# Kernel tuning notes

Measured on AMD Instinct MI355X. Metric: run time of the kernel, lower is better.

## Reference

```python
import jax, jax.numpy as jnp
import numpy as np

LN_EPS = 1e-5

def _layernorm(x, g, b):
    mu = jnp.mean(x, axis=-1, keepdims=True)
    var = jnp.var(x, axis=-1, keepdims=True)
    return (x - mu) * jax.lax.rsqrt(var + LN_EPS) * g + b

def setup_inputs() -> dict:
    key = jax.random.key(0)
    B, S, D, H = 2, 2048, 1024, 16
    dh = D // H          # 64
    r = 48               # r_attn = int(0.75*min(D,dh))
    r_out = 768          # int(0.75*D)
    I = 4 * D            # GPT-2 MLP inner dim
    r_mlp = 512          # int(0.5*min(D,I))
    ks = jax.random.split(key, 24)
    sc = lambda *sh: 0.02
    inp = {
        'hidden_states': jax.random.normal(ks[0], (B, S, D), jnp.float32),
        'ln1_g': jnp.ones((D,), jnp.float32), 'ln1_b': jnp.zeros((D,), jnp.float32),
        'ln2_g': jnp.ones((D,), jnp.float32), 'ln2_b': jnp.zeros((D,), jnp.float32),
        'q_U': jax.random.normal(ks[1], (D, H, r), jnp.float32) * 0.02,
        'q_V': jax.random.normal(ks[2], (H, r, dh), jnp.float32) * 0.02,
        'q_b': jax.random.normal(ks[3], (H, dh), jnp.float32) * 0.02,
        'k_U': jax.random.normal(ks[4], (D, H, r), jnp.float32) * 0.02,
        'k_V': jax.random.normal(ks[5], (H, r, dh), jnp.float32) * 0.02,
        'k_b': jax.random.normal(ks[6], (H, dh), jnp.float32) * 0.02,
        'v_U': jax.random.normal(ks[7], (D, H, r), jnp.float32) * 0.02,
        'v_V': jax.random.normal(ks[8], (H, r, dh), jnp.float32) * 0.02,
        'v_b': jax.random.normal(ks[9], (H, dh), jnp.float32) * 0.02,
        'out_U': jax.random.normal(ks[10], (D, r_out), jnp.float32) * 0.02,
        'out_V': jax.random.normal(ks[11], (r_out, D), jnp.float32) * 0.02,
        'out_b': jnp.zeros((D,), jnp.float32),
        'fc1_U': jax.random.normal(ks[12], (D, r_mlp), jnp.float32) * 0.02,
        'fc1_V': jax.random.normal(ks[13], (r_mlp, I), jnp.float32) * 0.02,
        'fc1_b': jnp.zeros((I,), jnp.float32),
        'fc2_U': jax.random.normal(ks[14], (I, r_mlp), jnp.float32) * 0.02,
        'fc2_V': jax.random.normal(ks[15], (r_mlp, D), jnp.float32) * 0.02,
        'fc2_b': jnp.zeros((D,), jnp.float32),
    }
    return inp

def reference(hidden_states, ln1_g, ln1_b, ln2_g, ln2_b,
              q_U, q_V, q_b, k_U, k_V, k_b, v_U, v_V, v_b,
              out_U, out_V, out_b, fc1_U, fc1_V, fc1_b, fc2_U, fc2_V, fc2_b):
    B, S, D = hidden_states.shape
    H, dh = q_V.shape[0], q_V.shape[2]
    x = _layernorm(hidden_states, ln1_g, ln1_b)
    # low-rank per-head projections (latent P then reconstruct)
    Q = jnp.einsum('bsd,dhr,hre->bhse', x, q_U, q_V) + q_b[None, :, None, :]
    Pk = jnp.einsum('bsd,dhr->bhsr', x, k_U)
    Pv = jnp.einsum('bsd,dhr->bhsr', x, v_U)
    K = jnp.einsum('bhsr,hrd->bhsd', Pk, k_V) + k_b[None, :, None, :]
    V = jnp.einsum('bhsr,hrd->bhsd', Pv, v_V) + v_b[None, :, None, :]
    # causal scaled dot-product attention
    scale = 1.0 / jnp.sqrt(jnp.asarray(dh, x.dtype))
    scores = jnp.einsum('bhse,bhte->bhst', Q, K) * scale
    causal = jnp.tril(jnp.ones((S, S), bool))
    scores = jnp.where(causal[None, None], scores, jnp.asarray(-1e9, scores.dtype))
    attn = jax.nn.softmax(scores, axis=-1)
    ctx = jnp.einsum('bhst,bhtd->bhsd', attn, V)          # [B,H,S,dh]
    ctx = ctx.transpose(0, 2, 1, 3).reshape(B, S, D)
    attn_out = (ctx @ out_U) @ out_V + out_b
    h = hidden_states + attn_out
    # low-rank MLP with GPT-2 gelu (tanh approx)
    x2 = _layernorm(h, ln2_g, ln2_b)
    hmid = jax.nn.gelu((x2 @ fc1_U) @ fc1_V + fc1_b, approximate=True)
    mlp_out = (hmid @ fc2_U) @ fc2_V + fc2_b
    return h + mlp_out
```

## Files before the change

kernel.cpp:

```cpp
#include <hip/hip_runtime.h>
#include <hip/hip_bf16.h>

typedef float f32x4 __attribute__((ext_vector_type(4)));
typedef __bf16 bf16x8 __attribute__((ext_vector_type(8)));
typedef __bf16 bf16x4 __attribute__((ext_vector_type(4)));
typedef unsigned short u16x8 __attribute__((ext_vector_type(8)));
typedef unsigned short u16x4 __attribute__((ext_vector_type(4)));

#define QSCALE 0.180336881f

__device__ __forceinline__ unsigned short f2bf(float f) {
  union { float f; unsigned int u; } v; v.f = f;
  return (unsigned short)((v.u + 0x7FFFu + ((v.u >> 16) & 1u)) >> 16);
}

__device__ __forceinline__ f32x4 mfma16(bf16x8 a, bf16x8 b, f32x4 c) {
  return __builtin_amdgcn_mfma_f32_16x16x32_bf16(a, b, c, 0, 0, 0);
}

__device__ __forceinline__ void gload16(const unsigned short* g, unsigned short* l) {
  __builtin_amdgcn_global_load_lds(
      (const __attribute__((address_space(1))) void*)g,
      (__attribute__((address_space(3))) void*)l, 16, 0, 0);
}


__global__ void concat_bias_k(const float* __restrict__ qb, const float* __restrict__ kb,
                              const float* __restrict__ vb, float* __restrict__ out) {
  const int i = blockIdx.x * 256 + threadIdx.x;
  if (i >= 3072) return;
  const float* s = (i < 1024) ? qb : (i < 2048 ? kb : vb);
  out[i] = s[i & 1023] * (i < 1024 ? QSCALE : 1.0f);
}

__global__ void tcvt_k(const float* __restrict__ in, unsigned short* __restrict__ out,
                       int R, int C) {
  __shared__ float tile[32][33];
  const int x = blockIdx.x * 32 + threadIdx.x;
  const int y0 = blockIdx.y * 32;
#pragma unroll
  for (int i = 0; i < 32; i += 8)
    tile[threadIdx.y + i][threadIdx.x] = in[(size_t)(y0 + threadIdx.y + i) * C + x];
  __syncthreads();
  const int ox = y0 + threadIdx.x;
  const int oy0 = blockIdx.x * 32;
#pragma unroll
  for (int i = 0; i < 32; i += 8)
    out[(size_t)(oy0 + threadIdx.y + i) * R + ox] = f2bf(tile[threadIdx.x][threadIdx.y + i]);
}

__global__ void cvt_k(const float* __restrict__ in, unsigned short* __restrict__ out, int n) {
  const int i = (blockIdx.x * 256 + threadIdx.x) * 4;
  if (i >= n) return;
  const f32x4 v = *(const f32x4*)(in + i);
  u16x4 o;
#pragma unroll
  for (int k = 0; k < 4; ++k) o[k] = f2bf(v[k]);
  *(u16x4*)(out + i) = o;
}

__global__ void vtr_k(const unsigned short* __restrict__ QKV, unsigned short* __restrict__ VT) {
  __shared__ unsigned short tile[32][33];
  const int bh = blockIdx.z, b = bh >> 4, h = bh & 15;
  const int s0 = blockIdx.x * 32, d0 = blockIdx.y * 32;
  const unsigned short* src = QKV + (size_t)b * 2048 * 3072 + 2048 + h * 64;
#pragma unroll
  for (int i = 0; i < 32; i += 8)
    tile[threadIdx.y + i][threadIdx.x] = src[(size_t)(s0 + threadIdx.y + i) * 3072 + d0 + threadIdx.x];
  __syncthreads();
  unsigned short* dst = VT + (size_t)bh * 64 * 2048;
#pragma unroll
  for (int i = 0; i < 32; i += 8)
    dst[(size_t)(d0 + threadIdx.y + i) * 2048 + s0 + threadIdx.x] = tile[threadIdx.x][threadIdx.y + i];
}

__global__ __launch_bounds__(256) void wqkv_pre_k(
    const float* __restrict__ qU, const float* __restrict__ qV,
    const float* __restrict__ kU, const float* __restrict__ kV,
    const float* __restrict__ vU, const float* __restrict__ vV,
    unsigned short* __restrict__ WT) {
  __shared__ float Us[64][48];
  __shared__ float Vs[48][64];
  const int m = blockIdx.y >> 4, h = blockIdx.y & 15;
  const int d0 = blockIdx.x * 64;
  const float* U = (m == 0) ? qU : (m == 1 ? kU : vU);
  const float* V = (m == 0) ? qV : (m == 1 ? kV : vV);
  const float qs = (m == 0) ? QSCALE : 1.0f;
  const int t = threadIdx.x;
  for (int idx = t; idx < 64 * 48; idx += 256) {
    const int d = idx / 48, r = idx - d * 48;
    Us[d][r] = U[(size_t)(d0 + d) * 768 + h * 48 + r];
  }
  for (int idx = t; idx < 48 * 64; idx += 256) {
    const int r = idx >> 6, e = idx & 63;
    Vs[r][e] = V[(h * 48 + r) * 64 + e];
  }
  __syncthreads();
  const int e = t & 63, dg = t >> 6;
  for (int j = 0; j < 16; ++j) {
    const int d = dg * 16 + j;
    float s = 0.f;
#pragma unroll
    for (int r = 0; r < 48; ++r) s = fmaf(Us[d][r], Vs[r][e], s);
    WT[(size_t)(m * 1024 + h * 64 + e) * 1024 + d0 + d] = f2bf(s * qs);
  }
}

__global__ __launch_bounds__(256) void ln_k(
    const float* __restrict__ in, const float* __restrict__ gw,
    const float* __restrict__ bw, unsigned short* __restrict__ out) {
  const int row = blockIdx.x, t = threadIdx.x;
  const f32x4 v = *(const f32x4*)(in + (size_t)row * 1024 + t * 4);
  float s = v[0] + v[1] + v[2] + v[3];
  float ss = v[0] * v[0] + v[1] * v[1] + v[2] * v[2] + v[3] * v[3];
#pragma unroll
  for (int off = 1; off < 64; off <<= 1) {
    s += __shfl_xor(s, off);
    ss += __shfl_xor(ss, off);
  }
  __shared__ float red[8];
  if ((t & 63) == 0) { red[(t >> 6) * 2] = s; red[(t >> 6) * 2 + 1] = ss; }
  __syncthreads();
  s = red[0] + red[2] + red[4] + red[6];
  ss = red[1] + red[3] + red[5] + red[7];
  const float mean = s * (1.0f / 1024.0f);
  const float rstd = rsqrtf(ss * (1.0f / 1024.0f) - mean * mean + 1e-5f);
  const f32x4 g4 = *(const f32x4*)(gw + t * 4);
  const f32x4 b4 = *(const f32x4*)(bw + t * 4);
  u16x4 o;
#pragma unroll
  for (int i = 0; i < 4; ++i) o[i] = f2bf((v[i] - mean) * rstd * g4[i] + b4[i]);
  *(u16x4*)(out + (size_t)row * 1024 + t * 4) = o;
}

__device__ __forceinline__ void xcd_swz(int& bx, int& by, int nx, int ny) {
  const int nwg = nx * ny;
  if ((nwg & 7) == 0) {
    const int d = by * nx + bx;
    const int k = (d & 7) * (nwg >> 3) + (d >> 3);
    bx = k % nx;
    by = k / nx;
  }
}

template <int BM, int BN, int EPI, int OUTBF>
__global__ __launch_bounds__(256) void gemm_k(
    const unsigned short* __restrict__ A, const unsigned short* __restrict__ Bt,
    const float* __restrict__ bias, const float* __restrict__ resid,
    void* __restrict__ Cout, int M, int N, int K) {
  constexpr int MI = BM / 32;
  constexpr int FN = BN / 32;
  constexpr int NL = (BM == 128 ? 2 : 1) + (BN == 128 ? 2 : 1);
  constexpr int SM_KLOOP = 3 * (BM + BN) * 32;
  constexpr int SM_EPI = OUTBF ? 4 * (BM / 2) * 72 : 0;
  constexpr int SME = SM_KLOOP > SM_EPI ? SM_KLOOP : SM_EPI;
  __shared__ unsigned short smem[SME];
  unsigned short* As = smem;
  unsigned short* Bs = smem + 3 * BM * 32;
  int bxi = blockIdx.x, byi = blockIdx.y;
  xcd_swz(bxi, byi, gridDim.x, gridDim.y);
  const int t = threadIdx.x;
  const int lane = t & 63, wid = t >> 6;
  const int m0 = byi * BM, n0 = bxi * BN;
  const int wm = (wid >> 1) * (BM / 2), wn = (wid & 1) * (BN / 2);
  const int fr = lane & 15, fg = (lane >> 4) * 8;

  f32x4 acc[MI][FN];
#pragma unroll
  for (int i = 0; i < MI; ++i)
#pragma unroll
    for (int j = 0; j < FN; ++j) acc[i][j] = (f32x4){0.f, 0.f, 0.f, 0.f};

  const unsigned short* Ag0 = A + (size_t)(m0 + (t >> 2)) * K + (t & 3) * 8;
  const unsigned short* Ag1 = A + (size_t)(m0 + 64 + (t >> 2)) * K + (t & 3) * 8;
  const unsigned short* Bg0 = Bt + (size_t)(n0 + (t >> 2)) * K + (t & 3) * 8;
  const unsigned short* Bg1 = Bt + (size_t)(n0 + 64 + (t >> 2)) * K + (t & 3) * 8;
  const int l0 = t * 8;

#define GEMM_STAGE(buf, ke)                                             \
  {                                                                     \
    gload16(Ag0 + (ke), &As[(buf) * BM * 32 + l0]);                     \
    if (BM == 128) gload16(Ag1 + (ke), &As[(buf) * BM * 32 + l0 + 2048]); \
    gload16(Bg0 + (ke), &Bs[(buf) * BN * 32 + l0]);                     \
    if (BN == 128) gload16(Bg1 + (ke), &Bs[(buf) * BN * 32 + l0 + 2048]); \
  }

  const int nk = K >> 5;
  GEMM_STAGE(0, 0);
  if (nk > 1) GEMM_STAGE(1, 32);

  int cur = 0, sb = 2;
  for (int kt = 0; kt < nk; ++kt) {
    if (kt + 1 < nk)
      asm volatile("s_waitcnt vmcnt(%0)" ::"n"(NL) : "memory");
    else
      asm volatile("s_waitcnt vmcnt(0)" ::: "memory");
    __builtin_amdgcn_s_barrier();
    __builtin_amdgcn_sched_barrier(0);
    if (kt + 2 < nk) GEMM_STAGE(sb, (kt + 2) * 32);
    bf16x8 af[MI], bfr[FN];
#pragma unroll
    for (int i = 0; i < MI; ++i)
      af[i] = *(const bf16x8*)&As[cur * BM * 32 + (wm + i * 16 + fr) * 32 + fg];
#pragma unroll
    for (int j = 0; j < FN; ++j)
      bfr[j] = *(const bf16x8*)&Bs[cur * BN * 32 + (wn + j * 16 + fr) * 32 + fg];
#pragma unroll
    for (int i = 0; i < MI; ++i)
#pragma unroll
      for (int j = 0; j < FN; ++j) acc[i][j] = mfma16(af[i], bfr[j], acc[i][j]);
    cur = (cur == 2) ? 0 : cur + 1;
    sb = (sb == 2) ? 0 : sb + 1;
  }
#undef GEMM_STAGE

  if (OUTBF) {
    __syncthreads();
    unsigned short* eb = smem + wid * ((BM / 2) * 72);
#pragma unroll
    for (int j = 0; j < FN; ++j) {
      const int colL = j * 16 + fr;
      const float bval = (EPI >= 1) ? bias[n0 + wn + colL] : 0.0f;
#pragma unroll
      for (int i = 0; i < MI; ++i) {
#pragma unroll
        for (int r = 0; r < 4; ++r) {
          const int rl = i * 16 + ((lane >> 4) << 2) + r;
          float v = acc[i][j][r] + bval;
          if (EPI == 2) {
            const float z = 0.7978845608028654f * (v + 0.044715f * v * v * v);
            v = v - v / (__expf(2.0f * z) + 1.0f);
          }
          eb[rl * 72 + colL] = f2bf(v);
        }
      }
    }
    __builtin_amdgcn_s_barrier();
    constexpr int CH = (BN / 2) / 8;
    constexpr int RPI = 64 / CH;
    const int c2 = lane % CH, r2b = lane / CH;
    unsigned short* Cg = (unsigned short*)Cout;
#pragma unroll
    for (int it = 0; it < (BM / 2) / RPI; ++it) {
      const int r2 = r2b + it * RPI;
      const u16x8 vv = *(const u16x8*)&eb[r2 * 72 + c2 * 8];
      *(u16x8*)&Cg[(size_t)(m0 + wm + r2) * N + n0 + wn + c2 * 8] = vv;
    }
  } else {
#pragma unroll
    for (int j = 0; j < FN; ++j) {
      const int col = n0 + wn + j * 16 + fr;
      const float bval = (EPI >= 1) ? bias[col] : 0.0f;
#pragma unroll
      for (int i = 0; i < MI; ++i) {
#pragma unroll
        for (int r = 0; r < 4; ++r) {
          const int row = m0 + wm + i * 16 + ((lane >> 4) << 2) + r;
          float v = acc[i][j][r] + bval;
          if (EPI == 3) v += resid[(size_t)row * N + col];
          ((float*)Cout)[(size_t)row * N + col] = v;
        }
      }
    }
  }
}

__global__ __launch_bounds__(512) void attn_k(
    const unsigned short* __restrict__ QKV, const unsigned short* __restrict__ VT,
    unsigned short* __restrict__ ctx) {
  __shared__ unsigned short Ks[2][64 * 64];
  __shared__ unsigned short Vs[2][64 * 64];
  __shared__ unsigned short Ps[8][16 * 64];
  int bxi = blockIdx.x, byi = blockIdx.y;
  xcd_swz(bxi, byi, 16, 32);
  const int qi = ((byi >> 1) & 1) ? (15 - bxi) : bxi;
  const int bh = byi, b = bh >> 4, h = bh & 15;
  const int nt = 2 * qi + 2;
  const int q0b = qi * 128;
  const int t = threadIdx.x, lane = t & 63, w = t >> 6;
  const int g = lane >> 4, c = lane & 15;
  const int cks = c & 7;
  const size_t base = (size_t)b * 2048 * 3072;

  const int r0 = t >> 3, ch0 = t & 7;
  const int lw = r0 * 64 + ((ch0 ^ (r0 & 7)) * 8);
  const unsigned short* Kg = QKV + base + 1024 + h * 64 + (size_t)r0 * 3072 + ch0 * 8;
  const unsigned short* Vg = VT + ((size_t)bh * 64 + r0) * 2048 + ch0 * 8;

  const int kro0 = (g ^ cks) * 8, kro1 = ((4 + g) ^ cks) * 8;

  bf16x8 onef;
#pragma unroll
  for (int i = 0; i < 8; ++i) onef[i] = (__bf16)1.0f;

  const int qrow = q0b + w * 16 + c;
  const unsigned short* qp = QKV + base + (size_t)qrow * 3072 + h * 64 + g * 8;
  const bf16x8 qf0 = *(const bf16x8*)qp;
  const bf16x8 qf1 = *(const bf16x8*)(qp + 32);

  f32x4 o[4];
#pragma unroll
  for (int d = 0; d < 4; ++d) o[d] = (f32x4){0.f, 0.f, 0.f, 0.f};
  f32x4 ol = (f32x4){0.f, 0.f, 0.f, 0.f};
  float mrow = -1e30f;

  u16x8 kr, vr;
#define ATTN_LOAD(kt_)                                        \
  {                                                           \
    kr = *(const u16x8*)(Kg + (size_t)(kt_) * 64 * 3072);     \
    vr = *(const u16x8*)(Vg + (kt_) * 64);                    \
  }
#define ATTN_WRITE(buf)                                       \
  {                                                           \
    *(u16x8*)&Ks[buf][lw] = kr;                               \
    *(u16x8*)&Vs[buf][lw] = vr;                               \
  }

  ATTN_LOAD(0);
  ATTN_WRITE(0);
  if (nt > 1) ATTN_LOAD(1);
  __syncthreads();

  const int fsrc = g * 20;

  for (int j = 0; j < nt; ++j) {
    const int cur = j & 1;
    const int kbase = j * 64;
    const bool active = (kbase <= q0b + w * 16 + 15);

    if (active) {
      f32x4 s4[4];
      __builtin_amdgcn_s_setprio(1);
#pragma unroll
      for (int t16 = 0; t16 < 4; ++t16) {
        const int krow = (t16 * 16 + c) * 64;
        const bf16x8 kf0 = *(const bf16x8*)&Ks[cur][krow + kro0];
        const bf16x8 kf1 = *(const bf16x8*)&Ks[cur][krow + kro1];
        f32x4 a = (f32x4){0.f, 0.f, 0.f, 0.f};
        a = mfma16(kf0, qf0, a);
        a = mfma16(kf1, qf1, a);
        s4[t16] = a;
      }
      __builtin_amdgcn_s_setprio(0);
      if (kbase + 63 > qrow) {
#pragma unroll
        for (int t16 = 0; t16 < 4; ++t16)
#pragma unroll
          for (int r = 0; r < 4; ++r)
            if (kbase + t16 * 16 + 4 * g + r > qrow) s4[t16][r] = -1e30f;
      }
      float mx = s4[0][0];
#pragma unroll
      for (int t16 = 0; t16 < 4; ++t16)
#pragma unroll
        for (int r = 0; r < 4; ++r) mx = fmaxf(mx, s4[t16][r]);
      mx = fmaxf(mx, __shfl_xor(mx, 16));
      mx = fmaxf(mx, __shfl_xor(mx, 32));
      const float mn = fmaxf(mrow, mx);
      const float fac = exp2f(mrow - mn);
      mrow = mn;
#pragma unroll
      for (int t16 = 0; t16 < 4; ++t16) {
        bf16x4 pw;
#pragma unroll
        for (int r = 0; r < 4; ++r) pw[r] = (__bf16)exp2f(s4[t16][r] - mrow);
        *(bf16x4*)&Ps[w][c * 64 + (((2 * t16 + (g >> 1)) ^ cks) * 8) + (g & 1) * 4] = pw;
      }
      float fo[4];
#pragma unroll
      for (int r = 0; r < 4; ++r) fo[r] = __shfl(fac, fsrc + r);
#pragma unroll
      for (int d = 0; d < 4; ++d)
#pragma unroll
        for (int r = 0; r < 4; ++r) o[d][r] *= fo[r];
#pragma unroll
      for (int r = 0; r < 4; ++r) ol[r] *= fo[r];
      __builtin_amdgcn_s_setprio(1);
#pragma unroll
      for (int ks = 0; ks < 2; ++ks) {
        const int po = ((ks * 4 + g) ^ cks) * 8;
        const bf16x8 pf = *(const bf16x8*)&Ps[w][c * 64 + po];
#pragma unroll
        for (int d = 0; d < 4; ++d) {
          const bf16x8 vf = *(const bf16x8*)&Vs[cur][(d * 16 + c) * 64 + po];
          o[d] = mfma16(pf, vf, o[d]);
        }
        ol = mfma16(pf, onef, ol);
      }
      __builtin_amdgcn_s_setprio(0);
    }

    if (j + 1 < nt) {
      __syncthreads();
      ATTN_WRITE(cur ^ 1);
      if (j + 2 < nt) ATTN_LOAD(j + 2);
      __syncthreads();
    }
  }
#pragma unroll
  for (int d = 0; d < 4; ++d)
#pragma unroll
    for (int r = 0; r < 4; ++r) {
      const float v = o[d][r] / ol[r];
      ctx[(size_t)(b * 2048 + q0b + w * 16 + g * 4 + r) * 1024 + h * 64 + d * 16 + c] = f2bf(v);
    }
#undef ATTN_LOAD
#undef ATTN_WRITE
}


extern "C" void kernel_launch(void* const* d_in, const int* in_sizes, int n_in,
                              void* d_out, int out_size, void* d_ws, size_t ws_size,
                              hipStream_t stream) {
  const float* hidden = (const float*)d_in[0];
  const float* ln1g = (const float*)d_in[1];
  const float* ln1b = (const float*)d_in[2];
  const float* ln2g = (const float*)d_in[3];
  const float* ln2b = (const float*)d_in[4];
  const float* qU = (const float*)d_in[5];
  const float* qV = (const float*)d_in[6];
  const float* qb = (const float*)d_in[7];
  const float* kU = (const float*)d_in[8];
  const float* kV = (const float*)d_in[9];
  const float* kb = (const float*)d_in[10];
  const float* vU = (const float*)d_in[11];
  const float* vV = (const float*)d_in[12];
  const float* vb = (const float*)d_in[13];
  const float* outU = (const float*)d_in[14];
  const float* outV = (const float*)d_in[15];
  const float* outb = (const float*)d_in[16];
  const float* fc1U = (const float*)d_in[17];
  const float* fc1V = (const float*)d_in[18];
  const float* fc1b = (const float*)d_in[19];
  const float* fc2U = (const float*)d_in[20];
  const float* fc2V = (const float*)d_in[21];
  const float* fc2b = (const float*)d_in[22];
  float* out = (float*)d_out;

  char* p = (char*)d_ws;
  unsigned short* x1x2 = (unsigned short*)p; p += (size_t)4096 * 1024 * 2;
  unsigned short* WqT_t1 = (unsigned short*)p; p += (size_t)3072 * 1024 * 2;
  float* bqkv = (float*)p; p += 3072 * 4;
  char* bigA = p; p += (size_t)4096 * 3072 * 2 + (size_t)4096 * 1024 * 2;
  unsigned short* QKV = (unsigned short*)bigA;
  unsigned short* ctxb = (unsigned short*)(bigA + (size_t)4096 * 3072 * 2);
  unsigned short* hmid = (unsigned short*)bigA;
  char* wo = p; p += (size_t)1024 * 768 * 2 * 2 + (size_t)1024 * 1024 * 2;
  unsigned short* outUb = (unsigned short*)wo;
  unsigned short* outVT = (unsigned short*)(wo + (size_t)1024 * 768 * 2);
  unsigned short* WoutT = (unsigned short*)(wo + (size_t)1024 * 768 * 2 * 2);
  unsigned short* t2 = (unsigned short*)wo;
  float* hbuf = (float*)p; p += (size_t)4096 * 1024 * 4;
  unsigned short* VT = (unsigned short*)hbuf;
  unsigned short* fc1UT = (unsigned short*)p; p += (size_t)512 * 1024 * 2;
  unsigned short* fc1VT = (unsigned short*)p; p += (size_t)4096 * 512 * 2;
  unsigned short* fc2UT = (unsigned short*)p; p += (size_t)512 * 4096 * 2;
  unsigned short* fc2VT = (unsigned short*)p; p += (size_t)1024 * 512 * 2;

  const dim3 b256(256);
  const dim3 tb(32, 8);

  concat_bias_k<<<12, b256, 0, stream>>>(qb, kb, vb, bqkv);
  wqkv_pre_k<<<dim3(16, 48), b256, 0, stream>>>(qU, qV, kU, kV, vU, vV, WqT_t1);
  tcvt_k<<<dim3(32, 24), tb, 0, stream>>>(outV, outVT, 768, 1024);
  cvt_k<<<768, b256, 0, stream>>>(outU, outUb, 1024 * 768);
  tcvt_k<<<dim3(16, 32), tb, 0, stream>>>(fc1U, fc1UT, 1024, 512);
  tcvt_k<<<dim3(128, 16), tb, 0, stream>>>(fc1V, fc1VT, 512, 4096);
  tcvt_k<<<dim3(16, 128), tb, 0, stream>>>(fc2U, fc2UT, 4096, 512);
  tcvt_k<<<dim3(32, 16), tb, 0, stream>>>(fc2V, fc2VT, 512, 1024);

  ln_k<<<4096, b256, 0, stream>>>(hidden, ln1g, ln1b, x1x2);
  gemm_k<128, 128, 1, 1><<<dim3(24, 32), b256, 0, stream>>>(x1x2, WqT_t1, bqkv, nullptr, QKV, 4096, 3072, 1024);
  vtr_k<<<dim3(64, 2, 32), tb, 0, stream>>>(QKV, VT);
  gemm_k<128, 128, 0, 1><<<dim3(8, 8), b256, 0, stream>>>(outVT, outUb, nullptr, nullptr, WoutT, 1024, 1024, 768);
  attn_k<<<dim3(16, 32), dim3(512), 0, stream>>>(QKV, VT, ctxb);
  gemm_k<64, 128, 3, 0><<<dim3(8, 64), b256, 0, stream>>>(ctxb, WoutT, outb, hidden, hbuf, 4096, 1024, 1024);

  ln_k<<<4096, b256, 0, stream>>>(hbuf, ln2g, ln2b, x1x2);
  gemm_k<64, 64, 0, 1><<<dim3(8, 64), b256, 0, stream>>>(x1x2, fc1UT, nullptr, nullptr, WqT_t1, 4096, 512, 1024);
  gemm_k<128, 128, 2, 1><<<dim3(32, 32), b256, 0, stream>>>(WqT_t1, fc1VT, fc1b, nullptr, hmid, 4096, 4096, 512);
  gemm_k<64, 64, 0, 1><<<dim3(8, 64), b256, 0, stream>>>(hmid, fc2UT, nullptr, nullptr, t2, 4096, 512, 4096);
  gemm_k<64, 128, 3, 0><<<dim3(8, 64), b256, 0, stream>>>(t2, fc2VT, fc2b, hbuf, out, 4096, 1024, 512);
}
```

Baseline: 258.8 us.

## Add 8-wave 128x128 GEMM for QKV and fc1; skip attention rescale when max stable

Adds a 512-thread GEMM variant in which eight waves share a 128x128 tile, each wave computing a 64x32 sub-tile, and uses it for the QKV projection and the fc1 reconstruction GEMM with GELU. This halves per-wave accumulator state and raises the number of waves available to hide latency. Separately, the attention softmax skips the running-max update and the rescaling of the output accumulators unless some row's new max exceeds the old one by more than 8 in log2 units. This is a lazy-rescale trick that cuts VALU work and shuffles per tile, at the cost of exponentials that can grow up to 2^8 before the rescale kicks in.

After: 253.3 us. -2.1%, faster.

```diff
diff --git a/kernel.cpp b/kernel.cpp
--- a/kernel.cpp
+++ b/kernel.cpp
@@ -143,6 +143,96 @@
   }
 }
 
+#define WVM(N) asm volatile("s_waitcnt vmcnt(%0)" ::"n"(N) : "memory")
+
+template <int EPI>
+__global__ __launch_bounds__(512) void gemm8_k(
+    const unsigned short* __restrict__ A, const unsigned short* __restrict__ Bt,
+    const float* __restrict__ bias, unsigned short* __restrict__ Cout,
+    int M, int N, int K) {
+  constexpr int ASZ = 128 * 32;
+  __shared__ unsigned short smem[6 * ASZ];
+  unsigned short* As = smem;
+  unsigned short* Bs = smem + 3 * ASZ;
+  int bxi = blockIdx.x, byi = blockIdx.y;
+  xcd_swz(bxi, byi, gridDim.x, gridDim.y);
+  const int t = threadIdx.x;
+  const int lane = t & 63, wid = t >> 6;
+  const int m0 = byi * 128, n0 = bxi * 128;
+  const int wm = (wid & 1) * 64, wn = (wid >> 1) * 32;
+  const int fr = lane & 15, fg = (lane >> 4) * 8;
+
+  f32x4 acc[4][2];
+#pragma unroll
+  for (int i = 0; i < 4; ++i)
+#pragma unroll
+    for (int j = 0; j < 2; ++j) acc[i][j] = (f32x4){0.f, 0.f, 0.f, 0.f};
+
+  const unsigned short* Ag = A + (size_t)(m0 + (t >> 2)) * K + (t & 3) * 8;
+  const unsigned short* Bg = Bt + (size_t)(n0 + (t >> 2)) * K + (t & 3) * 8;
+  const int l0 = t * 8;
+
+#define STG8(buf, ke)                          \
+  {                                            \
+    gload16(Ag + (ke), &As[(buf) * ASZ + l0]); \
+    gload16(Bg + (ke), &Bs[(buf) * ASZ + l0]); \
+  }
+
+  const int nk = K >> 5;
+  STG8(0, 0)
+  STG8(1, 32)
+
+  int cur = 0, sb = 2;
+  for (int kt = 0; kt < nk; ++kt) {
+    if (kt + 1 < nk) WVM(2); else WVM(0);
+    __builtin_amdgcn_s_barrier();
+    __builtin_amdgcn_sched_barrier(0);
+    if (kt + 2 < nk) STG8(sb, (kt + 2) * 32);
+    bf16x8 af[4], bf[2];
+#pragma unroll
+    for (int i = 0; i < 4; ++i)
+      af[i] = *(const bf16x8*)&As[cur * ASZ + (wm + i * 16 + fr) * 32 + fg];
+#pragma unroll
+    for (int j = 0; j < 2; ++j)
+      bf[j] = *(const bf16x8*)&Bs[cur * ASZ + (wn + j * 16 + fr) * 32 + fg];
+#pragma unroll
+    for (int i = 0; i < 4; ++i)
+#pragma unroll
+      for (int j = 0; j < 2; ++j) acc[i][j] = mfma16(af[i], bf[j], acc[i][j]);
+    cur = (cur == 2) ? 0 : cur + 1;
+    sb = (sb == 2) ? 0 : sb + 1;
+  }
+#undef STG8
+
+  __syncthreads();
+  unsigned short* eb = smem + wid * (64 * 40);
+#pragma unroll
+  for (int j = 0; j < 2; ++j) {
+    const int colL = j * 16 + fr;
+    const float bval = bias[n0 + wn + colL];
+#pragma unroll
+    for (int i = 0; i < 4; ++i) {
+#pragma unroll
+      for (int r = 0; r < 4; ++r) {
+        const int rl = i * 16 + ((lane >> 4) << 2) + r;
+        float v = acc[i][j][r] + bval;
+        if (EPI == 2) {
+          const float z = 0.7978845608028654f * (v + 0.044715f * v * v * v);
+          v = v - v / (__expf(2.0f * z) + 1.0f);
+        }
+        eb[rl * 40 + colL] = f2bf(v);
+      }
+    }
+  }
+  const int c2 = lane & 3, r2b = lane >> 2;
+#pragma unroll
+  for (int it = 0; it < 4; ++it) {
+    const int r2 = r2b + it * 16;
+    const u16x8 vv = *(const u16x8*)&eb[r2 * 40 + c2 * 8];
+    *(u16x8*)&Cout[(size_t)(m0 + wm + r2) * N + n0 + wn + c2 * 8] = vv;
+  }
+}
+
 template <int BM, int BN, int EPI, int OUTBF>
 __global__ __launch_bounds__(256) void gemm_k(
     const unsigned short* __restrict__ A, const unsigned short* __restrict__ Bt,
@@ -151,12 +241,13 @@
   constexpr int MI = BM / 32;
   constexpr int FN = BN / 32;
   constexpr int NL = (BM == 128 ? 2 : 1) + (BN == 128 ? 2 : 1);
-  constexpr int SM_KLOOP = 3 * (BM + BN) * 32;
+  constexpr int ASZ = BM * 32, BSZ = BN * 32;
+  constexpr int SM_KLOOP = 3 * (ASZ + BSZ);
   constexpr int SM_EPI = OUTBF ? 4 * (BM / 2) * 72 : 0;
   constexpr int SME = SM_KLOOP > SM_EPI ? SM_KLOOP : SM_EPI;
   __shared__ unsigned short smem[SME];
   unsigned short* As = smem;
-  unsigned short* Bs = smem + 3 * BM * 32;
+  unsigned short* Bs = smem + 3 * ASZ;
   int bxi = blockIdx.x, byi = blockIdx.y;
   xcd_swz(bxi, byi, gridDim.x, gridDim.y);
   const int t = threadIdx.x;
@@ -177,12 +268,12 @@
   const unsigned short* Bg1 = Bt + (size_t)(n0 + 64 + (t >> 2)) * K + (t & 3) * 8;
   const int l0 = t * 8;
 
-#define GEMM_STAGE(buf, ke)                                             \
-  {                                                                     \
-    gload16(Ag0 + (ke), &As[(buf) * BM * 32 + l0]);                     \
-    if (BM == 128) gload16(Ag1 + (ke), &As[(buf) * BM * 32 + l0 + 2048]); \
-    gload16(Bg0 + (ke), &Bs[(buf) * BN * 32 + l0]);                     \
-    if (BN == 128) gload16(Bg1 + (ke), &Bs[(buf) * BN * 32 + l0 + 2048]); \
+#define GEMM_STAGE(buf, ke)                                               \
+  {                                                                       \
+    gload16(Ag0 + (ke), &As[(buf) * ASZ + l0]);                           \
+    if (BM == 128) gload16(Ag1 + (ke), &As[(buf) * ASZ + l0 + 2048]);     \
+    gload16(Bg0 + (ke), &Bs[(buf) * BSZ + l0]);                           \
+    if (BN == 128) gload16(Bg1 + (ke), &Bs[(buf) * BSZ + l0 + 2048]);     \
   }
 
   const int nk = K >> 5;
@@ -192,19 +283,19 @@
   int cur = 0, sb = 2;
   for (int kt = 0; kt < nk; ++kt) {
     if (kt + 1 < nk)
-      asm volatile("s_waitcnt vmcnt(%0)" ::"n"(NL) : "memory");
+      WVM(NL);
     else
-      asm volatile("s_waitcnt vmcnt(0)" ::: "memory");
+      WVM(0);
     __builtin_amdgcn_s_barrier();
     __builtin_amdgcn_sched_barrier(0);
     if (kt + 2 < nk) GEMM_STAGE(sb, (kt + 2) * 32);
     bf16x8 af[MI], bfr[FN];
 #pragma unroll
     for (int i = 0; i < MI; ++i)
-      af[i] = *(const bf16x8*)&As[cur * BM * 32 + (wm + i * 16 + fr) * 32 + fg];
+      af[i] = *(const bf16x8*)&As[cur * ASZ + (wm + i * 16 + fr) * 32 + fg];
 #pragma unroll
     for (int j = 0; j < FN; ++j)
-      bfr[j] = *(const bf16x8*)&Bs[cur * BN * 32 + (wn + j * 16 + fr) * 32 + fg];
+      bfr[j] = *(const bf16x8*)&Bs[cur * BSZ + (wn + j * 16 + fr) * 32 + fg];
 #pragma unroll
     for (int i = 0; i < MI; ++i)
 #pragma unroll
@@ -356,9 +447,20 @@
         for (int r = 0; r < 4; ++r) mx = fmaxf(mx, s4[t16][r]);
       mx = fmaxf(mx, __shfl_xor(mx, 16));
       mx = fmaxf(mx, __shfl_xor(mx, 32));
-      const float mn = fmaxf(mrow, mx);
-      const float fac = exp2f(mrow - mn);
-      mrow = mn;
+      if (!__all(mx <= mrow + 8.0f)) {
+        const float mn = fmaxf(mrow, mx);
+        const float fac = exp2f(mrow - mn);
+        mrow = mn;
+        float fo[4];
+#pragma unroll
+        for (int r = 0; r < 4; ++r) fo[r] = __shfl(fac, fsrc + r);
+#pragma unroll
+        for (int d = 0; d < 4; ++d)
+#pragma unroll
+          for (int r = 0; r < 4; ++r) o[d][r] *= fo[r];
+#pragma unroll
+        for (int r = 0; r < 4; ++r) ol[r] *= fo[r];
+      }
 #pragma unroll
       for (int t16 = 0; t16 < 4; ++t16) {
         bf16x4 pw;
@@ -366,15 +468,6 @@
         for (int r = 0; r < 4; ++r) pw[r] = (__bf16)exp2f(s4[t16][r] - mrow);
         *(bf16x4*)&Ps[w][c * 64 + (((2 * t16 + (g >> 1)) ^ cks) * 8) + (g & 1) * 4] = pw;
       }
-      float fo[4];
-#pragma unroll
-      for (int r = 0; r < 4; ++r) fo[r] = __shfl(fac, fsrc + r);
-#pragma unroll
-      for (int d = 0; d < 4; ++d)
-#pragma unroll
-        for (int r = 0; r < 4; ++r) o[d][r] *= fo[r];
-#pragma unroll
-      for (int r = 0; r < 4; ++r) ol[r] *= fo[r];
       __builtin_amdgcn_s_setprio(1);
 #pragma unroll
       for (int ks = 0; ks < 2; ++ks) {
@@ -458,6 +551,7 @@
   unsigned short* fc2VT = (unsigned short*)p; p += (size_t)1024 * 512 * 2;
 
   const dim3 b256(256);
+  const dim3 b512(512);
   const dim3 tb(32, 8);
 
   concat_bias_k<<<12, b256, 0, stream>>>(qb, kb, vb, bqkv);
@@ -470,15 +564,15 @@
   tcvt_k<<<dim3(32, 16), tb, 0, stream>>>(fc2V, fc2VT, 512, 1024);
 
   ln_k<<<4096, b256, 0, stream>>>(hidden, ln1g, ln1b, x1x2);
-  gemm_k<128, 128, 1, 1><<<dim3(24, 32), b256, 0, stream>>>(x1x2, WqT_t1, bqkv, nullptr, QKV, 4096, 3072, 1024);
+  gemm8_k<1><<<dim3(24, 32), b512, 0, stream>>>(x1x2, WqT_t1, bqkv, QKV, 4096, 3072, 1024);
   vtr_k<<<dim3(64, 2, 32), tb, 0, stream>>>(QKV, VT);
   gemm_k<128, 128, 0, 1><<<dim3(8, 8), b256, 0, stream>>>(outVT, outUb, nullptr, nullptr, WoutT, 1024, 1024, 768);
-  attn_k<<<dim3(16, 32), dim3(512), 0, stream>>>(QKV, VT, ctxb);
+  attn_k<<<dim3(16, 32), b512, 0, stream>>>(QKV, VT, ctxb);
   gemm_k<64, 128, 3, 0><<<dim3(8, 64), b256, 0, stream>>>(ctxb, WoutT, outb, hidden, hbuf, 4096, 1024, 1024);
 
   ln_k<<<4096, b256, 0, stream>>>(hbuf, ln2g, ln2b, x1x2);
   gemm_k<64, 64, 0, 1><<<dim3(8, 64), b256, 0, stream>>>(x1x2, fc1UT, nullptr, nullptr, WqT_t1, 4096, 512, 1024);
-  gemm_k<128, 128, 2, 1><<<dim3(32, 32), b256, 0, stream>>>(WqT_t1, fc1VT, fc1b, nullptr, hmid, 4096, 4096, 512);
+  gemm8_k<2><<<dim3(32, 32), b512, 0, stream>>>(WqT_t1, fc1VT, fc1b, hmid, 4096, 4096, 512);
   gemm_k<64, 64, 0, 1><<<dim3(8, 64), b256, 0, stream>>>(hmid, fc2UT, nullptr, nullptr, t2, 4096, 512, 4096);
   gemm_k<64, 128, 3, 0><<<dim3(8, 64), b256, 0, stream>>>(t2, fc2VT, fc2b, hbuf, out, 4096, 1024, 512);
 }
```
